# Performance work log

Measured on AMD Instinct MI355X. Metric: run time of the kernel, lower is better.

## Reference

```python
import jax, jax.numpy as jnp
import numpy as np

NUM_BASE = 92
NUM_NOVEL = 40
GAMMA = 2.0
ALPHA = 0.25
DISTIL_FACTOR = 1.0
BSZ, N_DET, DIM_FEAT, DIM_HID, DIM_EMB = 16, 48, 2048, 1024, 512
EMB_HALF = DIM_EMB // 2


def _pair_ids(n):
    # all ordered pairs (i, j), i != j  (trajid2pairid)
    s, o = np.meshgrid(np.arange(n), np.arange(n), indexing='ij')
    m = s != o
    return s[m].astype(np.int32), o[m].astype(np.int32)


def _norm(x, eps=1e-12):
    # F.normalize(dim=-1)
    return x / jnp.maximum(jnp.linalg.norm(x, axis=-1, keepdims=True), eps)


def _sigmoid_focal_loss(logits, targets):
    # torchvision.ops.sigmoid_focal_loss, alpha=0.25, gamma=2, reduction='none'
    p = jax.nn.sigmoid(logits)
    ce = jnp.maximum(logits, 0) - logits * targets + jnp.log1p(jnp.exp(-jnp.abs(logits)))
    p_t = p * targets + (1.0 - p) * (1.0 - targets)
    loss = ce * (1.0 - p_t) ** GAMMA
    a_t = ALPHA * targets + (1.0 - ALPHA) * (1.0 - targets)
    return a_t * loss


def setup_inputs() -> dict:
    key = jax.random.key(0)
    ks = jax.random.split(key, 12)
    sids_np, oids_np = _pair_ids(N_DET)
    P = sids_np.shape[0]  # 2256 pairs per video
    w = lambda k, shape, s=0.02: jax.random.normal(k, shape, dtype=jnp.float32) * s
    return {
        'det_feats': jax.random.normal(ks[0], (BSZ, N_DET, DIM_FEAT), dtype=jnp.float32),
        'traj_embds': jax.random.normal(ks[1], (BSZ, N_DET, EMB_HALF), dtype=jnp.float32),
        'relpos_feats': jax.random.normal(ks[2], (BSZ, P, 12), dtype=jnp.float32),
        'classifier_weights': _norm(jax.random.normal(ks[3], (NUM_BASE, DIM_EMB), dtype=jnp.float32)) / np.sqrt(2.0),
        'W1': w(ks[4], (2 * DIM_FEAT, DIM_HID)), 'b1': jnp.zeros((DIM_HID,), jnp.float32),
        'W2': w(ks[5], (DIM_HID, DIM_HID)), 'b2': jnp.zeros((DIM_HID,), jnp.float32),
        'W3': w(ks[6], (DIM_HID, DIM_EMB)),
        'R1': w(ks[7], (12, 256), 0.1), 'rb1': jnp.zeros((256,), jnp.float32),
        'R2': w(ks[8], (256, DIM_EMB), 0.1),
        'temperature': jnp.full((1,), 0.02, dtype=jnp.float32),
        'labels': jax.random.randint(ks[9], (BSZ, P, 1 + NUM_BASE + NUM_NOVEL), 0, 2, dtype=jnp.int32),
        'sids': jnp.asarray(sids_np),
        'oids': jnp.asarray(oids_np),
    }


def reference(det_feats, traj_embds, relpos_feats, classifier_weights,
              W1, b1, W2, b2, W3, R1, rb1, R2, temperature,
              labels, sids, oids):
    Df = det_feats.shape[-1]
    De = traj_embds.shape[-1]
    # gather subject / object features for all pairs, flatten batch
    s_f = det_feats[:, sids, :].reshape(-1, Df)   # [N, Df]
    o_f = det_feats[:, oids, :].reshape(-1, Df)
    so = jnp.concatenate([s_f, o_f], axis=-1)      # [N, 2*Df]
    # trajpair_proj MLP
    h = jax.nn.relu(so @ W1 + b1)
    h = jax.nn.relu(h @ W2 + b2)
    so_proj = h @ W3                                # [N, dim_emb]
    so_n = _norm(so_proj)
    # relpos branch
    rp = relpos_feats.reshape(-1, relpos_feats.shape[-1])
    re = jax.nn.relu(rp @ R1 + rb1) @ R2
    re = _norm(re)
    combined = _norm(so_n + re)
    logits = (combined @ classifier_weights.T) / temperature  # [N, num_base]
    # cls_loss_on_base
    lab = labels.reshape(-1, 1 + NUM_BASE + NUM_NOVEL).astype(logits.dtype)
    pos_mask = jnp.any(lab[:, 1:1 + NUM_BASE] > 0, axis=-1)
    neg_mask = lab[:, 0] > 0
    lab_base = lab[:, 1:1 + NUM_BASE]
    fl_pos = _sigmoid_focal_loss(logits, lab_base)
    pos_den = jnp.maximum(pos_mask.sum(), 1).astype(logits.dtype) * NUM_BASE
    pos_loss = jnp.sum(fl_pos * pos_mask[:, None]) / pos_den
    fl_neg = _sigmoid_focal_loss(logits, jnp.zeros_like(logits))
    neg_den = jnp.maximum(neg_mask.sum(), 1).astype(logits.dtype) * NUM_BASE
    neg_loss = jnp.sum(fl_neg * neg_mask[:, None]) / neg_den
    # distillation L1 loss
    s_e = traj_embds[:, sids, :].reshape(-1, De)
    o_e = traj_embds[:, oids, :].reshape(-1, De)
    distil_target = jnp.concatenate([s_e, o_e], axis=-1)  # [N, dim_emb]
    distil_loss = jnp.mean(jnp.abs(distil_target - so_proj)) * DISTIL_FACTOR
    total_loss = pos_loss + neg_loss + distil_loss
    return total_loss
```

## Files before the change

kernel.cpp:

```cpp
#include <hip/hip_runtime.h>
#include <math.h>

constexpr int BSZ   = 16;
constexpr int NDET  = 48;
constexpr int PAIRS = NDET * (NDET - 1);
constexpr int ROWS  = BSZ * PAIRS;
constexpr int DF    = 2048;
constexpr int DH    = 1024;
constexpr int DE    = 512;
constexpr int EHALF = 256;
constexpr int NCLS  = 92;
constexpr int NEXT  = DE + 128;
constexpr int LABW  = 1 + 92 + 40;

typedef __attribute__((ext_vector_type(8))) short bf16x8;
typedef __attribute__((ext_vector_type(4))) float f32x4;

__device__ __forceinline__ short f2bf(float f) {
    union { float f; unsigned u; } a; a.f = f;
    unsigned r = a.u + 0x7fffu + ((a.u >> 16) & 1u);
    return (short)(r >> 16);
}
__device__ __forceinline__ float bf2f(short h) {
    union { unsigned u; float f; } x;
    x.u = ((unsigned)(unsigned short)h) << 16;
    return x.f;
}

constexpr int N4DET = BSZ * NDET * DF / 4;
constexpr int N4CWT = 128 * DE / 4;
constexpr int N4W3  = DH * DE / 4;
constexpr int N4R2  = 256 * DE / 4;
constexpr int NCONVB = (N4DET + N4CWT + N4W3 + N4R2) / 256;

struct TransJobs {
    const float* src[5];
    short*       dst[5];
    int K[5], N[5];
    int cum[6];
};

__global__ __launch_bounds__(256) void prep_kernel(
    const float* __restrict__ det, short* __restrict__ det_bf,
    const float* __restrict__ cw, short* __restrict__ cwt,
    const float* __restrict__ W3, short* __restrict__ W3bf,
    const float* __restrict__ R2, short* __restrict__ R2bf,
    TransJobs jobs)
{
    if (blockIdx.x < NCONVB) {
        int i = blockIdx.x * 256 + threadIdx.x;
        const float* src; short* dst; int k;
        if (i < N4DET) { src = det; dst = det_bf; k = i; }
        else if (i < N4DET + N4CWT) {
            k = i - N4DET;
            int n = (k * 4) >> 9;
            short4 o = {0, 0, 0, 0};
            if (n < NCLS) {
                float4 v = ((const float4*)cw)[k];
                o.x = f2bf(v.x); o.y = f2bf(v.y); o.z = f2bf(v.z); o.w = f2bf(v.w);
            }
            ((short4*)cwt)[k] = o;
            return;
        }
        else if (i < N4DET + N4CWT + N4W3) { src = W3; dst = W3bf; k = i - N4DET - N4CWT; }
        else { src = R2; dst = R2bf; k = i - N4DET - N4CWT - N4W3; }
        float4 v = ((const float4*)src)[k];
        short4 o;
        o.x = f2bf(v.x); o.y = f2bf(v.y); o.z = f2bf(v.z); o.w = f2bf(v.w);
        ((short4*)dst)[k] = o;
        return;
    }
    __shared__ float tile[32][33];
    int t = blockIdx.x - NCONVB;
    int j = 0;
    while (t >= jobs.cum[j + 1]) ++j;
    int lt = t - jobs.cum[j];
    int K = jobs.K[j], N = jobs.N[j];
    int nx = N >> 5;
    int ky = lt / nx, nxi = lt - ky * nx;
    int n0 = nxi * 32, k0 = ky * 32;
    const float* src = jobs.src[j];
    short* dst = jobs.dst[j];
    int tx = threadIdx.x & 31, ty = threadIdx.x >> 5;
#pragma unroll
    for (int i = ty; i < 32; i += 8)
        tile[i][tx] = src[(size_t)(k0 + i) * N + n0 + tx];
    __syncthreads();
#pragma unroll
    for (int i = ty; i < 32; i += 8)
        dst[(size_t)(n0 + i) * K + k0 + tx] = f2bf(tile[tx][i]);
}

__device__ __forceinline__ void load16_lds(const void* g, void* l) {
    __builtin_amdgcn_global_load_lds(
        (const __attribute__((address_space(1))) unsigned int*)g,
        (__attribute__((address_space(3))) unsigned int*)l, 16, 0, 0);
}

#define MFMA16 __builtin_amdgcn_mfma_f32_16x16x32_bf16

template <bool BIAS, bool RELU, bool OUTBF16, bool SWIZZLE, bool DUAL>
__global__ __launch_bounds__(256, 4) void mfma_gemm(
    const short* __restrict__ A, const short* __restrict__ Bt,
    const float* __restrict__ bias, void* __restrict__ C,
    int M, int N, int K, int lda, int ldb,
    const short* A2, const short* Bt2, void* C2, int nsplit,
    int K2, int lda2, int ldb2, int N2)
{
    __shared__ __align__(16) char smem_raw[32768];
    short* As = (short*)smem_raw;
    short* Bs = As + 128 * 64;

    int bx, by;
    if (SWIZZLE) {
        int nb  = gridDim.x;
        int gid = blockIdx.y * nb + blockIdx.x;
        int xcd = gid & 7;
        int j   = gid >> 3;
        int rows_per = gridDim.y >> 3;
        int lr  = j / nb;
        bx = j - lr * nb;
        by = xcd * rows_per + lr;
    } else {
        bx = blockIdx.x; by = blockIdx.y;
    }
    if (DUAL && bx >= nsplit) {
        bx -= nsplit; A = A2; Bt = Bt2; C = C2;
        K = K2; lda = lda2; ldb = ldb2; N = N2;
    }
    if (by * 128 >= M) return;

    const int tid  = threadIdx.x;
    const int wave = tid >> 6;
    const int lane = tid & 63;
    const int m0 = by * 128;
    const int n0 = bx * 128;
    const int wm = (wave & 1) * 64;
    const int wn = (wave >> 1) * 64;

    f32x4 acc[4][4] = {};

    const int q  = lane >> 4;
    const int lm = lane & 15;

    for (int k0 = 0; k0 < K; k0 += 64) {
#pragma unroll
        for (int it = 0; it < 4; ++it) {
            int c    = (it & 1) * 256 + tid;
            int half = it >> 1;
            int row  = c >> 2;
            int kk   = (c & 3) * 8 + half * 32;
            int ldsc = half * 4096 + ((it & 1) * 256 + wave * 64) * 8;
            int gm = m0 + row; if (gm >= M) gm = M - 1;
            load16_lds(A + (size_t)gm * lda + k0 + kk, As + ldsc);
            int gn = n0 + row;
            load16_lds(Bt + (size_t)gn * ldb + k0 + kk, Bs + ldsc);
        }
        __syncthreads();

#pragma unroll
        for (int half = 0; half < 2; ++half) {
            const short* Ah = As + half * 4096;
            const short* Bh = Bs + half * 4096;
            bf16x8 af[4], bfr[4];
#pragma unroll
            for (int t = 0; t < 4; ++t) {
                af[t]  = *(const bf16x8*)(Ah + (wm + t * 16 + lm) * 32 + q * 8);
                bfr[t] = *(const bf16x8*)(Bh + (wn + t * 16 + lm) * 32 + q * 8);
            }
#pragma unroll
            for (int tm = 0; tm < 4; ++tm)
#pragma unroll
                for (int tn = 0; tn < 4; ++tn)
                    acc[tm][tn] = MFMA16(af[tm], bfr[tn], acc[tm][tn], 0, 0, 0);
        }
        __syncthreads();
    }

    if (OUTBF16) {
        float* scratch = (float*)smem_raw + wave * (16 * 68);
#pragma unroll
        for (int tm = 0; tm < 4; ++tm) {
            __syncthreads();
#pragma unroll
            for (int tn = 0; tn < 4; ++tn) {
                float bv = BIAS ? bias[n0 + wn + tn * 16 + lm] : 0.0f;
#pragma unroll
                for (int r = 0; r < 4; ++r) {
                    float v = acc[tm][tn][r] + bv;
                    if (RELU) v = fmaxf(v, 0.0f);
                    scratch[(q * 4 + r) * 68 + tn * 16 + lm] = v;
                }
            }
            __syncthreads();
#pragma unroll
            for (int p = 0; p < 2; ++p) {
                int row16 = (lane >> 3) + p * 8;
                int c0 = (lane & 7) * 8;
                float4 v0 = *(float4*)&scratch[row16 * 68 + c0];
                float4 v1 = *(float4*)&scratch[row16 * 68 + c0 + 4];
                bf16x8 o;
                o[0] = f2bf(v0.x); o[1] = f2bf(v0.y); o[2] = f2bf(v0.z); o[3] = f2bf(v0.w);
                o[4] = f2bf(v1.x); o[5] = f2bf(v1.y); o[6] = f2bf(v1.z); o[7] = f2bf(v1.w);
                int grow = m0 + wm + tm * 16 + row16;
                if (grow < M)
                    *(bf16x8*)((short*)C + (size_t)grow * N + n0 + wn + c0) = o;
            }
        }
    } else {
#pragma unroll
        for (int tm = 0; tm < 4; ++tm)
#pragma unroll
            for (int tn = 0; tn < 4; ++tn) {
                int col = n0 + wn + tn * 16 + lm;
#pragma unroll
                for (int r = 0; r < 4; ++r) {
                    int row = m0 + wm + tm * 16 + q * 4 + r;
                    if (row < M) {
                        float v = acc[tm][tn][r];
                        if (BIAS) v += bias[col];
                        if (RELU) v = fmaxf(v, 0.0f);
                        ((float*)C)[(size_t)row * N + col] = v;
                    }
                }
            }
    }
}

__global__ __launch_bounds__(256, 3) void gemm_h2f(
    const short* __restrict__ UV,
    const int* __restrict__ sids, const int* __restrict__ oids,
    const short* __restrict__ Bt, const float* __restrict__ bias,
    short* __restrict__ C, int M, int rowbase)
{
    __shared__ __align__(16) char smem_raw[32768];
    short* As = (short*)smem_raw;
    short* Bs = As + 128 * 64;

    int nb  = gridDim.x;
    int gid = blockIdx.y * nb + blockIdx.x;
    int xcd = gid & 7;
    int j   = gid >> 3;
    int rows_per = gridDim.y >> 3;
    int lr  = j / nb;
    int bx = j - lr * nb;
    int by = xcd * rows_per + lr;
    if (by * 128 >= M) return;

    const int tid  = threadIdx.x;
    const int wave = tid >> 6;
    const int lane = tid & 63;
    const int m0 = by * 128;
    const int n0 = bx * 128;
    const int wm = (wave & 1) * 64;
    const int wn = (wave >> 1) * 64;

    const int cq = tid & 3;
    int lr0 = m0 + (tid >> 2); if (lr0 >= M) lr0 = M - 1;
    int lr1 = lr0 + 64;        if (lr1 >= M) lr1 = M - 1;
    int rg0 = rowbase + lr0, rg1 = rowbase + lr1;
    int b0 = rg0 / PAIRS, p0 = rg0 - b0 * PAIRS;
    int b1 = rg1 / PAIRS, p1 = rg1 - b1 * PAIRS;
    const short* u0 = UV + (size_t)(b0 * NDET + sids[p0]) * 2048;
    const short* v0 = UV + (size_t)(b0 * NDET + oids[p0]) * 2048 + 1024;
    const short* u1 = UV + (size_t)(b1 * NDET + sids[p1]) * 2048;
    const short* v1 = UV + (size_t)(b1 * NDET + oids[p1]) * 2048 + 1024;

    f32x4 acc[4][4] = {};
    const int q  = lane >> 4;
    const int lm = lane & 15;

    for (int k0 = 0; k0 < DH; k0 += 64) {
#pragma unroll
        for (int it = 0; it < 4; ++it) {
            int c    = (it & 1) * 256 + tid;
            int half = it >> 1;
            int row  = c >> 2;
            int kk   = (c & 3) * 8 + half * 32;
            int ldsc = half * 4096 + ((it & 1) * 256 + wave * 64) * 8;
            load16_lds(Bt + (size_t)(n0 + row) * DH + k0 + kk, Bs + ldsc);
        }
        int ka = k0 + cq * 8;
        bf16x8 ua0 = *(const bf16x8*)(u0 + ka),      va0 = *(const bf16x8*)(v0 + ka);
        bf16x8 ua1 = *(const bf16x8*)(u1 + ka),      va1 = *(const bf16x8*)(v1 + ka);
        bf16x8 ub0 = *(const bf16x8*)(u0 + ka + 32), vb0 = *(const bf16x8*)(v0 + ka + 32);
        bf16x8 ub1 = *(const bf16x8*)(u1 + ka + 32), vb1 = *(const bf16x8*)(v1 + ka + 32);
        bf16x8 w0, w1, w2, w3;
#pragma unroll
        for (int e = 0; e < 8; ++e) {
            w0[e] = f2bf(fmaxf(bf2f(ua0[e]) + bf2f(va0[e]), 0.0f));
            w1[e] = f2bf(fmaxf(bf2f(ua1[e]) + bf2f(va1[e]), 0.0f));
            w2[e] = f2bf(fmaxf(bf2f(ub0[e]) + bf2f(vb0[e]), 0.0f));
            w3[e] = f2bf(fmaxf(bf2f(ub1[e]) + bf2f(vb1[e]), 0.0f));
        }
        *(bf16x8*)(As + tid * 8)                = w0;
        *(bf16x8*)(As + (256 + tid) * 8)        = w1;
        *(bf16x8*)(As + 4096 + tid * 8)         = w2;
        *(bf16x8*)(As + 4096 + (256 + tid) * 8) = w3;
        __syncthreads();

#pragma unroll
        for (int half = 0; half < 2; ++half) {
            const short* Ah = As + half * 4096;
            const short* Bh = Bs + half * 4096;
            bf16x8 af[4], bfr[4];
#pragma unroll
            for (int t = 0; t < 4; ++t) {
                af[t]  = *(const bf16x8*)(Ah + (wm + t * 16 + lm) * 32 + q * 8);
                bfr[t] = *(const bf16x8*)(Bh + (wn + t * 16 + lm) * 32 + q * 8);
            }
#pragma unroll
            for (int tm = 0; tm < 4; ++tm)
#pragma unroll
                for (int tn = 0; tn < 4; ++tn)
                    acc[tm][tn] = MFMA16(af[tm], bfr[tn], acc[tm][tn], 0, 0, 0);
        }
        __syncthreads();
    }

    float* scratch = (float*)smem_raw + wave * (16 * 68);
#pragma unroll
    for (int tm = 0; tm < 4; ++tm) {
        __syncthreads();
#pragma unroll
        for (int tn = 0; tn < 4; ++tn) {
            float bv = bias[n0 + wn + tn * 16 + lm];
#pragma unroll
            for (int r = 0; r < 4; ++r) {
                float v = fmaxf(acc[tm][tn][r] + bv, 0.0f);
                scratch[(q * 4 + r) * 68 + tn * 16 + lm] = v;
            }
        }
        __syncthreads();
#pragma unroll
        for (int p = 0; p < 2; ++p) {
            int row16 = (lane >> 3) + p * 8;
            int c0 = (lane & 7) * 8;
            float4 x0 = *(float4*)&scratch[row16 * 68 + c0];
            float4 x1 = *(float4*)&scratch[row16 * 68 + c0 + 4];
            bf16x8 o;
            o[0] = f2bf(x0.x); o[1] = f2bf(x0.y); o[2] = f2bf(x0.z); o[3] = f2bf(x0.w);
            o[4] = f2bf(x1.x); o[5] = f2bf(x1.y); o[6] = f2bf(x1.z); o[7] = f2bf(x1.w);
            int grow = m0 + wm + tm * 16 + row16;
            if (grow < M)
                *(bf16x8*)(C + (size_t)grow * DH + n0 + wn + c0) = o;
        }
    }
}

struct GemmJobs {
    const short* A[4]; const short* Bt[4]; short* C[4];
    int M[4], N[4], K[4], lda[4], ldb[4];
    int cum[5];
};

__global__ __launch_bounds__(256, 4) void mfma_gemm_multi(GemmJobs jobs)
{
    __shared__ __align__(16) char smem_raw[32768];
    short* As = (short*)smem_raw;
    short* Bs = As + 128 * 64;

    int bid = blockIdx.x;
    int j = 0;
    while (bid >= jobs.cum[j + 1]) ++j;
    int lt = bid - jobs.cum[j];
    const short* A  = jobs.A[j];
    const short* Bt = jobs.Bt[j];
    short* C = jobs.C[j];
    int M = jobs.M[j], N = jobs.N[j], K = jobs.K[j];
    int lda = jobs.lda[j], ldb = jobs.ldb[j];
    int ncols = N >> 7;
    int by = lt / ncols;
    int bx = lt - by * ncols;

    const int tid  = threadIdx.x;
    const int wave = tid >> 6;
    const int lane = tid & 63;
    const int m0 = by * 128;
    const int n0 = bx * 128;
    const int wm = (wave & 1) * 64;
    const int wn = (wave >> 1) * 64;

    f32x4 acc[4][4] = {};
    const int q  = lane >> 4;
    const int lm = lane & 15;

    for (int k0 = 0; k0 < K; k0 += 64) {
#pragma unroll
        for (int it = 0; it < 4; ++it) {
            int c    = (it & 1) * 256 + tid;
            int half = it >> 1;
            int row  = c >> 2;
            int kk   = (c & 3) * 8 + half * 32;
            int ldsc = half * 4096 + ((it & 1) * 256 + wave * 64) * 8;
            int gm = m0 + row; if (gm >= M) gm = M - 1;
            load16_lds(A + (size_t)gm * lda + k0 + kk, As + ldsc);
            load16_lds(Bt + (size_t)(n0 + row) * ldb + k0 + kk, Bs + ldsc);
        }
        __syncthreads();
#pragma unroll
        for (int half = 0; half < 2; ++half) {
            const short* Ah = As + half * 4096;
            const short* Bh = Bs + half * 4096;
            bf16x8 af[4], bfr[4];
#pragma unroll
            for (int t = 0; t < 4; ++t) {
                af[t]  = *(const bf16x8*)(Ah + (wm + t * 16 + lm) * 32 + q * 8);
                bfr[t] = *(const bf16x8*)(Bh + (wn + t * 16 + lm) * 32 + q * 8);
            }
#pragma unroll
            for (int tm = 0; tm < 4; ++tm)
#pragma unroll
                for (int tn = 0; tn < 4; ++tn)
                    acc[tm][tn] = MFMA16(af[tm], bfr[tn], acc[tm][tn], 0, 0, 0);
        }
        __syncthreads();
    }

    float* scratch = (float*)smem_raw + wave * (16 * 68);
#pragma unroll
    for (int tm = 0; tm < 4; ++tm) {
        __syncthreads();
#pragma unroll
        for (int tn = 0; tn < 4; ++tn)
#pragma unroll
            for (int r = 0; r < 4; ++r)
                scratch[(q * 4 + r) * 68 + tn * 16 + lm] = acc[tm][tn][r];
        __syncthreads();
#pragma unroll
        for (int p = 0; p < 2; ++p) {
            int row16 = (lane >> 3) + p * 8;
            int c0 = (lane & 7) * 8;
            float4 v0 = *(float4*)&scratch[row16 * 68 + c0];
            float4 v1 = *(float4*)&scratch[row16 * 68 + c0 + 4];
            bf16x8 o;
            o[0] = f2bf(v0.x); o[1] = f2bf(v0.y); o[2] = f2bf(v0.z); o[3] = f2bf(v0.w);
            o[4] = f2bf(v1.x); o[5] = f2bf(v1.y); o[6] = f2bf(v1.z); o[7] = f2bf(v1.w);
            int grow = m0 + wm + tm * 16 + row16;
            if (grow < M)
                *(bf16x8*)(C + (size_t)grow * N + n0 + wn + c0) = o;
        }
    }
}

constexpr int N4UV = BSZ * NDET * 2048 / 4;
__global__ __launch_bounds__(256) void uvmerge_kernel(
    short* __restrict__ UVa, const short* __restrict__ UVb,
    const float* __restrict__ b1)
{
    int i = blockIdx.x * 256 + threadIdx.x;
    if (i >= N4UV) return;
    short4 a = ((const short4*)UVa)[i];
    short4 b = ((const short4*)UVb)[i];
    int col4 = i & 511;
    float4 bb = {0.0f, 0.0f, 0.0f, 0.0f};
    if (col4 < 256) bb = ((const float4*)b1)[col4];
    short4 o;
    o.x = f2bf(bf2f(a.x) + bf2f(b.x) + bb.x);
    o.y = f2bf(bf2f(a.y) + bf2f(b.y) + bb.y);
    o.z = f2bf(bf2f(a.z) + bf2f(b.z) + bb.z);
    o.w = f2bf(bf2f(a.w) + bf2f(b.w) + bb.w);
    ((short4*)UVa)[i] = o;
}

__global__ __launch_bounds__(256) void rh_kernel(
    const float* __restrict__ rp, const float* __restrict__ R1,
    const float* __restrict__ rb1, short* __restrict__ rh, int b0)
{
    int wave = threadIdx.x >> 6, lane = threadIdx.x & 63;
    int r = blockIdx.x * 4 + wave;
    int rg = b0 * PAIRS + r;

    const float* rowp = rp + (size_t)rg * 12;
    float4 acc = ((const float4*)rb1)[lane];
#pragma unroll
    for (int k = 0; k < 12; ++k) {
        float rv = rowp[k];
        float4 w = ((const float4*)(R1 + k * 256))[lane];
        acc.x = fmaf(rv, w.x, acc.x);
        acc.y = fmaf(rv, w.y, acc.y);
        acc.z = fmaf(rv, w.z, acc.z);
        acc.w = fmaf(rv, w.w, acc.w);
    }
    short4 o;
    o.x = f2bf(fmaxf(acc.x, 0.0f));
    o.y = f2bf(fmaxf(acc.y, 0.0f));
    o.z = f2bf(fmaxf(acc.z, 0.0f));
    o.w = f2bf(fmaxf(acc.w, 0.0f));
    ((short4*)(rh + (size_t)r * 256))[lane] = o;
}

__global__ __launch_bounds__(256) void rowprep_focal_kernel(
    const short* __restrict__ so_ext, const short* __restrict__ re_ext,
    const float* __restrict__ traj, const float* __restrict__ temperature,
    const int* __restrict__ sids, const int* __restrict__ oids,
    const int* __restrict__ labels,
    float4* __restrict__ pn, float* __restrict__ dist_arr, int b0)
{
    int wave = threadIdx.x >> 6, lane = threadIdx.x & 63;
    int r = blockIdx.x * 4 + wave;
    int rg = b0 * PAIRS + r;
    int b = b0 + r / PAIRS;
    int p = r % PAIRS;

    const short* srow = so_ext + (size_t)r * NEXT;
    const short* rrow = re_ext + (size_t)r * NEXT;
    bf16x8 sv = *(const bf16x8*)(srow + lane * 8);
    bf16x8 uv = *(const bf16x8*)(rrow + lane * 8);
    float s[8], u[8];
#pragma unroll
    for (int i = 0; i < 8; ++i) { s[i] = bf2f(sv[i]); u[i] = bf2f(uv[i]); }

    const float* tsrc = (lane < 32)
        ? (traj + (size_t)(b * NDET + sids[p]) * EHALF + lane * 8)
        : (traj + (size_t)(b * NDET + oids[p]) * EHALF + (lane - 32) * 8);
    float4 t0 = ((const float4*)tsrc)[0], t1 = ((const float4*)tsrc)[1];
    float t[8] = {t0.x, t0.y, t0.z, t0.w, t1.x, t1.y, t1.z, t1.w};

    float ss = 0.0f, sr = 0.0f, rho = 0.0f, sd = 0.0f;
#pragma unroll
    for (int i = 0; i < 8; ++i) {
        ss  += s[i] * s[i];
        sr  += u[i] * u[i];
        rho += s[i] * u[i];
        sd  += fabsf(t[i] - s[i]);
    }
#pragma unroll
    for (int m = 1; m < 64; m <<= 1) {
        ss  += __shfl_xor(ss, m);
        sr  += __shfl_xor(sr, m);
        rho += __shfl_xor(rho, m);
        sd  += __shfl_xor(sd, m);
    }
    float inv_s = 1.0f / fmaxf(sqrtf(ss), 1e-12f);
    float inv_r = 1.0f / fmaxf(sqrtf(sr), 1e-12f);
    float ncomb = sqrtf(fmaxf(2.0f + 2.0f * rho * inv_s * inv_r, 0.0f));
    float scale = 1.0f / (fmaxf(ncomb, 1e-12f) * temperature[0]);

    float flp = 0.0f, fln = 0.0f, fm = 0.0f;
    size_t labbase = (size_t)rg * LABW;
#pragma unroll
    for (int h = 0; h < 2; ++h) {
        int c = lane + h * 64;
        if (c < NCLS) {
            float l = (bf2f(srow[DE + c]) * inv_s + bf2f(rrow[DE + c]) * inv_r) * scale;
            int tl = labels[labbase + 1 + c];
            if (tl > 0) fm = 1.0f;
            float tf = (float)tl;
            float pr = 1.0f / (1.0f + expf(-l));
            float lg = log1pf(expf(-fabsf(l)));
            float ce = fmaxf(l, 0.0f) - l * tf + lg;
            float pt = pr * tf + (1.0f - pr) * (1.0f - tf);
            float om = 1.0f - pt;
            float at = 0.25f * tf + 0.75f * (1.0f - tf);
            flp += at * ce * om * om;
            float ce0 = fmaxf(l, 0.0f) + lg;
            fln += 0.75f * ce0 * pr * pr;
        }
    }
#pragma unroll
    for (int m = 1; m < 64; m <<= 1) {
        flp += __shfl_xor(flp, m);
        fln += __shfl_xor(fln, m);
        fm  += __shfl_xor(fm, m);
    }
    if (lane == 0) {
        int posf = (fm > 0.5f) ? 1 : 0;
        int negf = (labels[labbase] > 0) ? 1 : 0;
        pn[rg] = make_float4(posf ? flp : 0.0f, negf ? fln : 0.0f, 0.0f,
                             (float)(posf + 2 * negf));
        dist_arr[rg] = sd;
    }
}

struct RedRec { double sp, sn, sd; int cp, cn; };
constexpr int RED1 = 64;
constexpr int ROWS_PER_RED = ROWS / RED1;

__global__ __launch_bounds__(256) void reduce1_kernel(
    const float4* __restrict__ pn, const float* __restrict__ dist_arr,
    RedRec* __restrict__ scratch)
{
    int tid = threadIdx.x;
    int base = blockIdx.x * ROWS_PER_RED;
    double sp = 0.0, sn = 0.0, sd = 0.0;
    int cp = 0, cn = 0;
    for (int i = tid; i < ROWS_PER_RED; i += 256) {
        float4 v = pn[base + i];
        sp += (double)v.x; sn += (double)v.y; sd += (double)dist_arr[base + i];
        int f = (int)v.w;
        cp += f & 1; cn += (f >> 1) & 1;
    }
    __shared__ double A[256], B[256], C[256];
    __shared__ int I[256], J[256];
    A[tid] = sp; B[tid] = sn; C[tid] = sd; I[tid] = cp; J[tid] = cn;
    __syncthreads();
    for (int st = 128; st > 0; st >>= 1) {
        if (tid < st) { A[tid] += A[tid + st]; B[tid] += B[tid + st]; C[tid] += C[tid + st];
                        I[tid] += I[tid + st]; J[tid] += J[tid + st]; }
        __syncthreads();
    }
    if (tid == 0) {
        RedRec rec; rec.sp = A[0]; rec.sn = B[0]; rec.sd = C[0];
        rec.cp = I[0]; rec.cn = J[0];
        scratch[blockIdx.x] = rec;
    }
}

__global__ __launch_bounds__(64) void reduce2_kernel(
    const RedRec* __restrict__ scratch, float* __restrict__ out)
{
    int lane = threadIdx.x;
    RedRec rec = scratch[lane];
    double sp = rec.sp, sn = rec.sn, sd = rec.sd;
    int cp = rec.cp, cn = rec.cn;
#pragma unroll
    for (int m = 1; m < 64; m <<= 1) {
        sp += __shfl_xor(sp, m);
        sn += __shfl_xor(sn, m);
        sd += __shfl_xor(sd, m);
        cp += __shfl_xor(cp, m);
        cn += __shfl_xor(cn, m);
    }
    if (lane == 0) {
        int cpv = cp < 1 ? 1 : cp;
        int cnv = cn < 1 ? 1 : cn;
        out[0] = (float)(sp / ((double)cpv * NCLS) +
                         sn / ((double)cnv * NCLS) +
                         sd / ((double)ROWS * DE));
    }
}

static inline int pad8(int x) { return (x + 7) & ~7; }

extern "C" void kernel_launch(void* const* d_in, const int* in_sizes, int n_in,
                              void* d_out, int out_size, void* d_ws, size_t ws_size,
                              hipStream_t stream)
{
    const float* det    = (const float*)d_in[0];
    const float* traj   = (const float*)d_in[1];
    const float* relpos = (const float*)d_in[2];
    const float* cw     = (const float*)d_in[3];
    const float* W1     = (const float*)d_in[4];
    const float* b1     = (const float*)d_in[5];
    const float* W2     = (const float*)d_in[6];
    const float* b2     = (const float*)d_in[7];
    const float* W3     = (const float*)d_in[8];
    const float* R1     = (const float*)d_in[9];
    const float* rb1    = (const float*)d_in[10];
    const float* R2     = (const float*)d_in[11];
    const float* temp   = (const float*)d_in[12];
    const int*   labels = (const int*)d_in[13];
    const int*   sids   = (const int*)d_in[14];
    const int*   oids   = (const int*)d_in[15];
    float* out = (float*)d_out;

    char* ws = (char*)d_ws;
    size_t off = 0;
    auto carve = [&](size_t bytes) -> char* {
        char* p = ws + off;
        off = (off + bytes + 255) & ~(size_t)255;
        return p;
    };
    float4* pn       = (float4*)carve((size_t)ROWS * 16);
    float*  dist_arr = (float*)carve((size_t)ROWS * 4);
    short*  det_bf   = (short*)carve((size_t)BSZ * NDET * DF * 2);
    short*  W1t      = (short*)carve((size_t)2048 * 2048 * 2);
    short*  W2t      = (short*)carve((size_t)DH * DH * 2);
    short*  W3t      = (short*)carve((size_t)NEXT * DH * 2);
    short*  R2t      = (short*)carve((size_t)NEXT * 256 * 2);
    short*  cwt      = (short*)carve((size_t)128 * DE * 2);
    short*  W3bf     = (short*)carve((size_t)DH * DE * 2);
    short*  R2bf     = (short*)carve((size_t)256 * DE * 2);
    short*  UVa      = (short*)carve((size_t)BSZ * NDET * 2048 * 2);
    short*  UVb      = (short*)carve((size_t)BSZ * NDET * 2048 * 2);
    RedRec* red_scratch = (RedRec*)carve((size_t)RED1 * sizeof(RedRec));
    size_t fixed_off = off;

    int b_ch = 1;
    for (int cand : {16, 8, 4, 2, 1}) {
        size_t rows  = (size_t)cand * PAIRS;
        size_t bytes = fixed_off + rows * 2048 + 256 + rows * 2048 + 256
                     + rows * 512 + 256 + rows * 1280 + 256;
        if (bytes <= ws_size) { b_ch = cand; break; }
    }
    const int chunk_rows = b_ch * PAIRS;
    const int n_chunks = BSZ / b_ch;
    char* reg1 = carve((size_t)chunk_rows * 2048);
    char* reg2 = carve((size_t)chunk_rows * 2048);
    char* reg3 = carve((size_t)chunk_rows * 512);
    char* reg4 = carve((size_t)chunk_rows * 1280);

    short* h2     = (short*)reg2;
    short* so_ext = (short*)reg1;
    short* rh     = (short*)reg3;
    short* re_ext = (short*)reg4;

    TransJobs tj;
    tj.src[0] = W1;                    tj.dst[0] = W1t;                   tj.K[0] = DF;  tj.N[0] = DH;
    tj.src[1] = W1 + (size_t)DF * DH;  tj.dst[1] = W1t + (size_t)DH * DF; tj.K[1] = DF;  tj.N[1] = DH;
    tj.src[2] = W2;                    tj.dst[2] = W2t;                   tj.K[2] = DH;  tj.N[2] = DH;
    tj.src[3] = W3;                    tj.dst[3] = W3t;                   tj.K[3] = DH;  tj.N[3] = DE;
    tj.src[4] = R2;                    tj.dst[4] = R2t;                   tj.K[4] = 256; tj.N[4] = DE;
    tj.cum[0] = 0;
    for (int i = 0; i < 5; ++i)
        tj.cum[i + 1] = tj.cum[i] + (tj.K[i] / 32) * (tj.N[i] / 32);
    prep_kernel<<<NCONVB + tj.cum[5], 256, 0, stream>>>(
        det, det_bf, cw, cwt, W3, W3bf, R2, R2bf, tj);

    GemmJobs gj;
    gj.A[0] = det_bf;        gj.Bt[0] = W1t;        gj.C[0] = UVa;
    gj.M[0] = BSZ * NDET;    gj.N[0] = 2048;        gj.K[0] = 1024;
    gj.lda[0] = 2048;        gj.ldb[0] = 2048;
    gj.A[1] = det_bf + 1024; gj.Bt[1] = W1t + 1024; gj.C[1] = UVb;
    gj.M[1] = BSZ * NDET;    gj.N[1] = 2048;        gj.K[1] = 1024;
    gj.lda[1] = 2048;        gj.ldb[1] = 2048;
    gj.A[2] = cwt;           gj.Bt[2] = W3bf;       gj.C[2] = W3t + (size_t)512 * DH;
    gj.M[2] = 128;           gj.N[2] = 1024;        gj.K[2] = 512;
    gj.lda[2] = 512;         gj.ldb[2] = 512;
    gj.A[3] = cwt;           gj.Bt[3] = R2bf;       gj.C[3] = R2t + (size_t)512 * 256;
    gj.M[3] = 128;           gj.N[3] = 256;         gj.K[3] = 512;
    gj.lda[3] = 512;         gj.ldb[3] = 512;
    gj.cum[0] = 0;
    for (int i = 0; i < 4; ++i)
        gj.cum[i + 1] = gj.cum[i] + (gj.N[i] / 128) * ((gj.M[i] + 127) / 128);
    mfma_gemm_multi<<<gj.cum[4], 256, 0, stream>>>(gj);

    uvmerge_kernel<<<(N4UV + 255) / 256, 256, 0, stream>>>(UVa, UVb, b1);

    const int mg  = (chunk_rows + 127) / 128;
    const int mgp = pad8(mg);

    for (int c = 0; c < n_chunks; ++c) {
        int b0 = c * b_ch;

        rh_kernel<<<chunk_rows / 4, 256, 0, stream>>>(
            relpos, R1, rb1, rh, b0);

        gemm_h2f<<<dim3(DH / 128, mgp), 256, 0, stream>>>(
            UVa, sids, oids, W2t, b2, h2, chunk_rows, b0 * PAIRS);

        mfma_gemm<false, false, true, true, true>
            <<<dim3(10, mgp), 256, 0, stream>>>(
            h2, W3t, nullptr, so_ext, chunk_rows, NEXT, DH, DH, DH,
            rh, R2t, re_ext, 5, 256, 256, 256, NEXT);

        rowprep_focal_kernel<<<chunk_rows / 4, 256, 0, stream>>>(
            so_ext, re_ext, traj, temp, sids, oids, labels, pn, dist_arr, b0);
    }

    reduce1_kernel<<<RED1, 256, 0, stream>>>(pn, dist_arr, red_scratch);
    reduce2_kernel<<<1, 64, 0, stream>>>(red_scratch, out);
}
```

Before: 385.7 us.

## Widen gemm_h2f N-tile to 256 to halve gathered A-operand recomputation

Each gemm_h2f block now computes a 128x256 output tile instead of 128x128: every wave owns 64x128 with 32 accumulators, and B tiles for two 128-column subblocks are staged in 48KB LDS. This halves the number of blocks that gather UV rows and recompute add+relu+bf16 conversion of the A operand. It also swaps the scalar bf16 rounding in that conversion for the packed v_cvt_pk_bf16_f32 instruction. The cost is more registers and LDS per block, so launch bounds drop to 2 waves/SIMD and the grid has half as many blocks, which lowers occupancy.

```diff
diff --git a/kernel.cpp b/kernel.cpp
--- a/kernel.cpp
+++ b/kernel.cpp
@@ -227,13 +227,30 @@
     }
 }
 
-__global__ __launch_bounds__(256, 3) void gemm_h2f(
+__device__ __forceinline__ unsigned cvtpk(float lo, float hi) {
+    unsigned r;
+    asm("v_cvt_pk_bf16_f32 %0, %1, %2" : "=v"(r) : "v"(lo), "v"(hi));
+    return r;
+}
+__device__ __forceinline__ bf16x8 addrelu_pack(bf16x8 u, bf16x8 v) {
+    float f[8];
+#pragma unroll
+    for (int e = 0; e < 8; ++e)
+        f[e] = fmaxf(bf2f(u[e]) + bf2f(v[e]), 0.0f);
+    union { unsigned w[4]; bf16x8 o; } r;
+#pragma unroll
+    for (int j = 0; j < 4; ++j)
+        r.w[j] = cvtpk(f[2 * j], f[2 * j + 1]);
+    return r.o;
+}
+
+__global__ __launch_bounds__(256, 2) void gemm_h2f(
     const short* __restrict__ UV,
     const int* __restrict__ sids, const int* __restrict__ oids,
     const short* __restrict__ Bt, const float* __restrict__ bias,
     short* __restrict__ C, int M, int rowbase)
 {
-    __shared__ __align__(16) char smem_raw[32768];
+    __shared__ __align__(16) char smem_raw[49152];
     short* As = (short*)smem_raw;
     short* Bs = As + 128 * 64;
 
@@ -251,9 +268,9 @@
     const int wave = tid >> 6;
     const int lane = tid & 63;
     const int m0 = by * 128;
-    const int n0 = bx * 128;
-    const int wm = (wave & 1) * 64;
-    const int wn = (wave >> 1) * 64;
+    const int n0 = bx * 256;
+    const int wm   = (wave & 1) * 64;
+    const int wsub = wave >> 1;
 
     const int cq = tid & 3;
     int lr0 = m0 + (tid >> 2); if (lr0 >= M) lr0 = M - 1;
@@ -266,84 +283,84 @@
     const short* u1 = UV + (size_t)(b1 * NDET + sids[p1]) * 2048;
     const short* v1 = UV + (size_t)(b1 * NDET + oids[p1]) * 2048 + 1024;
 
-    f32x4 acc[4][4] = {};
+    f32x4 acc[4][8] = {};
     const int q  = lane >> 4;
     const int lm = lane & 15;
 
     for (int k0 = 0; k0 < DH; k0 += 64) {
 #pragma unroll
-        for (int it = 0; it < 4; ++it) {
-            int c    = (it & 1) * 256 + tid;
-            int half = it >> 1;
-            int row  = c >> 2;
-            int kk   = (c & 3) * 8 + half * 32;
-            int ldsc = half * 4096 + ((it & 1) * 256 + wave * 64) * 8;
-            load16_lds(Bt + (size_t)(n0 + row) * DH + k0 + kk, Bs + ldsc);
-        }
+        for (int sub = 0; sub < 2; ++sub)
+#pragma unroll
+            for (int it = 0; it < 4; ++it) {
+                int c    = (it & 1) * 256 + tid;
+                int half = it >> 1;
+                int row  = c >> 2;
+                int kk   = (c & 3) * 8 + half * 32;
+                int ldsc = sub * 8192 + half * 4096 + ((it & 1) * 256 + wave * 64) * 8;
+                load16_lds(Bt + (size_t)(n0 + sub * 128 + row) * DH + k0 + kk,
+                           Bs + ldsc);
+            }
         int ka = k0 + cq * 8;
-        bf16x8 ua0 = *(const bf16x8*)(u0 + ka),      va0 = *(const bf16x8*)(v0 + ka);
-        bf16x8 ua1 = *(const bf16x8*)(u1 + ka),      va1 = *(const bf16x8*)(v1 + ka);
-        bf16x8 ub0 = *(const bf16x8*)(u0 + ka + 32), vb0 = *(const bf16x8*)(v0 + ka + 32);
-        bf16x8 ub1 = *(const bf16x8*)(u1 + ka + 32), vb1 = *(const bf16x8*)(v1 + ka + 32);
-        bf16x8 w0, w1, w2, w3;
-#pragma unroll
-        for (int e = 0; e < 8; ++e) {
-            w0[e] = f2bf(fmaxf(bf2f(ua0[e]) + bf2f(va0[e]), 0.0f));
-            w1[e] = f2bf(fmaxf(bf2f(ua1[e]) + bf2f(va1[e]), 0.0f));
-            w2[e] = f2bf(fmaxf(bf2f(ub0[e]) + bf2f(vb0[e]), 0.0f));
-            w3[e] = f2bf(fmaxf(bf2f(ub1[e]) + bf2f(vb1[e]), 0.0f));
-        }
-        *(bf16x8*)(As + tid * 8)                = w0;
-        *(bf16x8*)(As + (256 + tid) * 8)        = w1;
-        *(bf16x8*)(As + 4096 + tid * 8)         = w2;
-        *(bf16x8*)(As + 4096 + (256 + tid) * 8) = w3;
+        *(bf16x8*)(As + tid * 8) =
+            addrelu_pack(*(const bf16x8*)(u0 + ka), *(const bf16x8*)(v0 + ka));
+        *(bf16x8*)(As + (256 + tid) * 8) =
+            addrelu_pack(*(const bf16x8*)(u1 + ka), *(const bf16x8*)(v1 + ka));
+        *(bf16x8*)(As + 4096 + tid * 8) =
+            addrelu_pack(*(const bf16x8*)(u0 + ka + 32), *(const bf16x8*)(v0 + ka + 32));
+        *(bf16x8*)(As + 4096 + (256 + tid) * 8) =
+            addrelu_pack(*(const bf16x8*)(u1 + ka + 32), *(const bf16x8*)(v1 + ka + 32));
         __syncthreads();
 
 #pragma unroll
         for (int half = 0; half < 2; ++half) {
             const short* Ah = As + half * 4096;
-            const short* Bh = Bs + half * 4096;
-            bf16x8 af[4], bfr[4];
-#pragma unroll
-            for (int t = 0; t < 4; ++t) {
-                af[t]  = *(const bf16x8*)(Ah + (wm + t * 16 + lm) * 32 + q * 8);
-                bfr[t] = *(const bf16x8*)(Bh + (wn + t * 16 + lm) * 32 + q * 8);
-            }
+            const short* Bh = Bs + wsub * 8192 + half * 4096;
+            bf16x8 af[4], bfr[8];
+#pragma unroll
+            for (int t = 0; t < 4; ++t)
+                af[t] = *(const bf16x8*)(Ah + (wm + t * 16 + lm) * 32 + q * 8);
+#pragma unroll
+            for (int t = 0; t < 8; ++t)
+                bfr[t] = *(const bf16x8*)(Bh + (t * 16 + lm) * 32 + q * 8);
 #pragma unroll
             for (int tm = 0; tm < 4; ++tm)
 #pragma unroll
-                for (int tn = 0; tn < 4; ++tn)
+                for (int tn = 0; tn < 8; ++tn)
                     acc[tm][tn] = MFMA16(af[tm], bfr[tn], acc[tm][tn], 0, 0, 0);
         }
         __syncthreads();
     }
 
-    float* scratch = (float*)smem_raw + wave * (16 * 68);
+    float* scratch = (float*)smem_raw + wave * (16 * 132);
+    const int csub = n0 + wsub * 128;
 #pragma unroll
     for (int tm = 0; tm < 4; ++tm) {
         __syncthreads();
 #pragma unroll
-        for (int tn = 0; tn < 4; ++tn) {
-            float bv = bias[n0 + wn + tn * 16 + lm];
+        for (int tn = 0; tn < 8; ++tn) {
+            float bv = bias[csub + tn * 16 + lm];
 #pragma unroll
             for (int r = 0; r < 4; ++r) {
                 float v = fmaxf(acc[tm][tn][r] + bv, 0.0f);
-                scratch[(q * 4 + r) * 68 + tn * 16 + lm] = v;
+                scratch[(q * 4 + r) * 132 + tn * 16 + lm] = v;
             }
         }
         __syncthreads();
 #pragma unroll
         for (int p = 0; p < 2; ++p) {
             int row16 = (lane >> 3) + p * 8;
-            int c0 = (lane & 7) * 8;
-            float4 x0 = *(float4*)&scratch[row16 * 68 + c0];
-            float4 x1 = *(float4*)&scratch[row16 * 68 + c0 + 4];
-            bf16x8 o;
-            o[0] = f2bf(x0.x); o[1] = f2bf(x0.y); o[2] = f2bf(x0.z); o[3] = f2bf(x0.w);
-            o[4] = f2bf(x1.x); o[5] = f2bf(x1.y); o[6] = f2bf(x1.z); o[7] = f2bf(x1.w);
-            int grow = m0 + wm + tm * 16 + row16;
-            if (grow < M)
-                *(bf16x8*)(C + (size_t)grow * DH + n0 + wn + c0) = o;
+            int grow  = m0 + wm + tm * 16 + row16;
+            if (grow >= M) continue;
+#pragma unroll
+            for (int cc = 0; cc < 2; ++cc) {
+                int c0 = (lane & 7) * 16 + cc * 8;
+                float4 x0 = *(float4*)&scratch[row16 * 132 + c0];
+                float4 x1 = *(float4*)&scratch[row16 * 132 + c0 + 4];
+                bf16x8 o;
+                o[0] = f2bf(x0.x); o[1] = f2bf(x0.y); o[2] = f2bf(x0.z); o[3] = f2bf(x0.w);
+                o[4] = f2bf(x1.x); o[5] = f2bf(x1.y); o[6] = f2bf(x1.z); o[7] = f2bf(x1.w);
+                *(bf16x8*)(C + (size_t)grow * DH + csub + c0) = o;
+            }
         }
     }
 }
@@ -737,7 +754,7 @@
         rh_kernel<<<chunk_rows / 4, 256, 0, stream>>>(
             relpos, R1, rb1, rh, b0);
 
-        gemm_h2f<<<dim3(DH / 128, mgp), 256, 0, stream>>>(
+        gemm_h2f<<<dim3(DH / 256, mgp), 256, 0, stream>>>(
             UVa, sids, oids, W2t, b2, h2, chunk_rows, b0 * PAIRS);
 
         mfma_gemm<false, false, true, true, true>
```

After: 383.5 us. No clear change (-0.6%).
